# Kernel tuning notes

Measured on AMD Instinct MI355X. Metric: run time of the kernel, lower is better.

Reference implementation:

```python
import jax, jax.numpy as jnp
import numpy as np

DIM = 512
HEADS = 8
ALPHA = 0.5
HIDDEN = int(DIM * 2.0)
EPS = 1e-5


def _layernorm(x, g, b):
    mu = jnp.mean(x, axis=-1, keepdims=True)
    var = jnp.var(x, axis=-1, keepdims=True)
    return (x - mu) * jax.lax.rsqrt(var + EPS) * g + b


def setup_inputs() -> dict:
    key = jax.random.key(0)
    ks = jax.random.split(key, 8)
    B, N, C = 4, 1536, DIM
    s = lambda fan_in: 1.0 / np.sqrt(fan_in)
    return {
        "x": jax.random.normal(ks[0], (B, N, C), dtype=jnp.float32),
        "ln1_g": jnp.ones((C,), jnp.float32),
        "ln1_b": jnp.zeros((C,), jnp.float32),
        "qkv_w": jax.random.normal(ks[1], (C, 3 * C), jnp.float32) * s(C),
        "qkv_b": jnp.zeros((3 * C,), jnp.float32),
        "ln2_g": jnp.ones((C,), jnp.float32),
        "ln2_b": jnp.zeros((C,), jnp.float32),
        "fc1_w": jax.random.normal(ks[2], (C, HIDDEN), jnp.float32) * s(C),
        "fc1_b": jnp.zeros((HIDDEN,), jnp.float32),
        "fc2_w": jax.random.normal(ks[3], (HIDDEN, C), jnp.float32) * s(HIDDEN),
        "fc2_b": jnp.zeros((C,), jnp.float32),
    }


def reference(x, ln1_g, ln1_b, qkv_w, qkv_b, ln2_g, ln2_b, fc1_w, fc1_b, fc2_w, fc2_b):
    B, N, C = x.shape
    H = HEADS
    d = C // H
    S = N // 3

    h = _layernorm(x, ln1_g, ln1_b)
    qkv = (h @ qkv_w + qkv_b).reshape(B, N, 3, H, d)
    qkv = jnp.transpose(qkv, (2, 0, 3, 1, 4))  # [3,B,H,N,d]
    q, k, v = qkv[0], qkv[1], qkv[2]

    attn = jnp.einsum('bhnd,bhmd->bhnm', q, k) * (d ** -0.5)  # [B,H,N,N]
    # sequential cross-segment score mixing (matches in-place torch semantics)
    s0 = attn[:, :, 0:S]
    s1 = attn[:, :, S:2 * S] + ALPHA * s0
    s2 = attn[:, :, 2 * S:] + ALPHA * s1
    attn = jnp.concatenate([s0, s1, s2], axis=2)
    attn = jax.nn.softmax(attn, axis=-1)

    o = jnp.einsum('bhnm,bhmd->bhnd', attn, v)
    o = jnp.transpose(o, (0, 2, 1, 3)).reshape(B, N, C)
    x = x + o  # NOTE: self.proj is defined but unused in the original forward

    h2 = _layernorm(x, ln2_g, ln2_b)
    m = jax.nn.gelu(h2 @ fc1_w + fc1_b, approximate=False) @ fc2_w + fc2_b
    return x + m
```

## Files before the change

### kernel.cpp

```cpp
#include <hip/hip_runtime.h>
#include <hip/hip_bf16.h>
#include <math.h>

#define DIMC 512
#define NSEQ 1536
#define BATCH 4
#define NHEADS 8
#define HDIM 64
#define SSEG 512
#define HIDDEN_DIM 1024
#define ALPHA_C 0.5f
#define EPS_C 1e-5f
#define NROWS (BATCH*NSEQ)
#define SHIFT_L2 8.65617025f
#define HSHIFT_L2 4.328085125f
#define QSCALE_L2 0.18033688f

typedef __attribute__((ext_vector_type(8))) short bfrag8;
typedef __attribute__((ext_vector_type(8))) _Float16 hfrag8;
typedef __attribute__((ext_vector_type(2))) __fp16 h2;
typedef __attribute__((ext_vector_type(4))) float ffrag;
typedef float4 f4;


__device__ __forceinline__ ushort f2bf(float v) {
    __hip_bfloat16 hb = __float2bfloat16(v);
    return *(ushort*)&hb;
}

__device__ __forceinline__ void gl2lds16(const ushort* g, ushort* l) {
    __builtin_amdgcn_global_load_lds(
        (const __attribute__((address_space(1))) unsigned*)g,
        (__attribute__((address_space(3))) unsigned*)l, 16, 0, 0);
}

__global__ __launch_bounds__(256)
void prep_kernel(const float* __restrict__ qkv_w, const float* __restrict__ fc1_w,
                 const float* __restrict__ fc2_w, ushort* __restrict__ qkv_wt,
                 ushort* __restrict__ fc1_wt, ushort* __restrict__ fc2_wt,
                 const float* __restrict__ x, const float* __restrict__ g,
                 const float* __restrict__ bvec, ushort* __restrict__ h_out)
{
    int bid = blockIdx.x;
    if (bid < 448) {
        __shared__ float tile[64][65];
        const float* W; ushort* Wt; int K, N, n0, k0;
        if (bid < 192)      { W = qkv_w; Wt = qkv_wt; K = 512;  N = 1536; int b = bid;       n0 = (b % 24) * 64; k0 = (b / 24) * 64; }
        else if (bid < 320) { W = fc1_w; Wt = fc1_wt; K = 512;  N = 1024; int b = bid - 192; n0 = (b % 16) * 64; k0 = (b / 16) * 64; }
        else                { W = fc2_w; Wt = fc2_wt; K = 1024; N = 512;  int b = bid - 320; n0 = (b % 8)  * 64; k0 = (b / 8)  * 64; }
        int tx = threadIdx.x & 63, ty = threadIdx.x >> 6;
        #pragma unroll
        for (int i = 0; i < 16; i++) {
            int r = i * 4 + ty;
            tile[r][tx] = W[(size_t)(k0 + r) * N + n0 + tx];
        }
        __syncthreads();
        #pragma unroll
        for (int i = 0; i < 16; i++) {
            int r = i * 4 + ty;
            Wt[(size_t)(n0 + r) * K + k0 + tx] = f2bf(tile[tx][r]);
        }
    } else {
        __shared__ float red[16];
        int row = bid - 448;
        int t = threadIdx.x;
        int lane = t & 63, w = t >> 6;
        const float* rp = x + (size_t)row * DIMC;
        float v0 = rp[t];
        float v1 = rp[t + 256];
        float s = v0 + v1;
        float s2 = v0 * v0 + v1 * v1;
        #pragma unroll
        for (int o = 32; o > 0; o >>= 1) {
            s  += __shfl_down(s,  o, 64);
            s2 += __shfl_down(s2, o, 64);
        }
        if (lane == 0) { red[w] = s; red[8 + w] = s2; }
        __syncthreads();
        if (t == 0) {
            float a = red[0] + red[1] + red[2] + red[3];
            float c = red[8] + red[9] + red[10] + red[11];
            red[0] = a; red[8] = c;
        }
        __syncthreads();
        float mean = red[0] * (1.0f / DIMC);
        float var  = red[8] * (1.0f / DIMC) - mean * mean;
        float rstd = rsqrtf(var + EPS_C);
        ushort* op = h_out + (size_t)row * DIMC;
        op[t]       = f2bf((v0 - mean) * rstd * g[t]       + bvec[t]);
        op[t + 256] = f2bf((v1 - mean) * rstd * g[t + 256] + bvec[t + 256]);
    }
}

__global__ __launch_bounds__(256)
void ln_kernel(const float* __restrict__ in, const float* __restrict__ g,
               const float* __restrict__ b, ushort* __restrict__ out)
{
    __shared__ float red[16];
    int row = blockIdx.x;
    int t = threadIdx.x;
    int lane = t & 63, w = t >> 6;
    const float* rp = in + (size_t)row * DIMC;
    float v0 = rp[t];
    float v1 = rp[t + 256];
    float s = v0 + v1;
    float s2 = v0 * v0 + v1 * v1;
    #pragma unroll
    for (int o = 32; o > 0; o >>= 1) {
        s  += __shfl_down(s,  o, 64);
        s2 += __shfl_down(s2, o, 64);
    }
    if (lane == 0) { red[w] = s; red[8 + w] = s2; }
    __syncthreads();
    if (t == 0) {
        float a = red[0] + red[1] + red[2] + red[3];
        float c = red[8] + red[9] + red[10] + red[11];
        red[0] = a; red[8] = c;
    }
    __syncthreads();
    float mean = red[0] * (1.0f / DIMC);
    float var  = red[8] * (1.0f / DIMC) - mean * mean;
    float rstd = rsqrtf(var + EPS_C);
    ushort* op = out + (size_t)row * DIMC;
    op[t]       = f2bf((v0 - mean) * rstd * g[t]       + b[t]);
    op[t + 256] = f2bf((v1 - mean) * rstd * g[t + 256] + b[t + 256]);
}

template <int EPI>
__device__ __forceinline__
void mgemm_body(const ushort* __restrict__ A, const ushort* __restrict__ Wt,
                const float* __restrict__ bias, const float* resid,
                void* out, int M, int K, int Nn, int bx, int by,
                ushort* As, ushort* Bs)
{
    int tid = threadIdx.x;
    int lane = tid & 63, w = tid >> 6;
    int cl = lane & 15, qg = lane >> 4;
    int wm = w >> 1, wn = w & 1;
    int rowBase = by * 64, colBase = bx * 64;
    int sr = lane >> 2;
    int sb = (lane & 3) * 8;

    const ushort* agb = A  + (size_t)(rowBase + w * 16 + sr) * K + sb;
    const ushort* bgb = Wt + (size_t)(colBase + w * 16 + sr) * K + sb;

    ffrag acc[2][2];
    #pragma unroll
    for (int mi = 0; mi < 2; mi++)
        #pragma unroll
        for (int ni = 0; ni < 2; ni++)
            #pragma unroll
            for (int r = 0; r < 4; r++) acc[mi][ni][r] = 0.f;

    int niter = K >> 6;

    #pragma unroll
    for (int hf = 0; hf < 2; hf++) {
        gl2lds16(agb + hf * 32, As + (0 * 2 + hf) * 2048 + (w * 16) * 32);
        gl2lds16(bgb + hf * 32, Bs + (0 * 2 + hf) * 2048 + (w * 16) * 32);
    }
    __syncthreads();

    for (int it = 0; it < niter; it++) {
        int cur = it & 1;
        if (it + 1 < niter) {
            int k0 = (it + 1) * 64;
            #pragma unroll
            for (int hf = 0; hf < 2; hf++) {
                gl2lds16(agb + k0 + hf * 32, As + ((cur ^ 1) * 2 + hf) * 2048 + (w * 16) * 32);
                gl2lds16(bgb + k0 + hf * 32, Bs + ((cur ^ 1) * 2 + hf) * 2048 + (w * 16) * 32);
            }
        }
        #pragma unroll
        for (int ks = 0; ks < 2; ks++) {
            bfrag8 af[2], bf[2];
            #pragma unroll
            for (int mi = 0; mi < 2; mi++)
                af[mi] = *(const bfrag8*)&As[(cur * 2 + ks) * 2048 + (wm * 32 + mi * 16 + cl) * 32 + qg * 8];
            #pragma unroll
            for (int ni = 0; ni < 2; ni++)
                bf[ni] = *(const bfrag8*)&Bs[(cur * 2 + ks) * 2048 + (wn * 32 + ni * 16 + cl) * 32 + qg * 8];
            #pragma unroll
            for (int mi = 0; mi < 2; mi++)
                #pragma unroll
                for (int ni = 0; ni < 2; ni++)
                    acc[mi][ni] = __builtin_amdgcn_mfma_f32_16x16x32_bf16(af[mi], bf[ni], acc[mi][ni], 0, 0, 0);
        }
        if (it + 1 < niter) __syncthreads();
    }

    int bb = (EPI == 3) ? (colBase / 1536) : 0;

    #pragma unroll
    for (int mi = 0; mi < 2; mi++) {
        #pragma unroll
        for (int ni = 0; ni < 2; ni++) {
            #pragma unroll
            for (int r = 0; r < 4; r++) {
                int row = rowBase + wm * 32 + mi * 16 + qg * 4 + r;
                int col = colBase + wn * 32 + ni * 16 + cl;
                float v = acc[mi][ni][r] + (EPI == 3 ? bias[row] : bias[col]);
                if (EPI == 0 && col < DIMC) v *= QSCALE_L2;
                if (EPI == 1) v = 0.5f * v * (1.0f + erff(v * 0.70710678118654752f));
                if (EPI == 2) {
                    v += resid[(size_t)row * Nn + col];
                    ((float*)out)[(size_t)row * Nn + col] = v;
                } else if (EPI == 3) {
                    int t = col - bb * 1536;
                    int h = row >> 6, dl = row & 63;
                    int t32 = t & 31;
                    int slot = ((t32 & 15) >> 2) * 8 + (t32 >> 4) * 4 + (t32 & 3);
                    size_t a = ((size_t)(bb * 8 + h) * 48 + (t >> 5)) * 2048
                             + (dl >> 4) * 512 + (dl & 15) * 32 + slot;
                    _Float16 e = (_Float16)v;
                    ((ushort*)out)[a] = *(ushort*)&e;
                } else {
                    ((ushort*)out)[(size_t)row * Nn + col] = f2bf(v);
                }
            }
        }
    }
}

template <int EPI>
__device__ __forceinline__
void mgemm128_body(const ushort* __restrict__ A, const ushort* __restrict__ Wt,
                   const float* __restrict__ bias, void* out, void* out2,
                   int K, int Nn, int bx, int by,
                   ushort* As, ushort* Bs)
{
    int tid = threadIdx.x;
    int lane = tid & 63, w = tid >> 6;
    int cl = lane & 15, qg = lane >> 4;
    int wm = w >> 1, wn = w & 1;
    int rowBase = by * 64, colBase = bx * 128;
    int sr = lane >> 2;
    int sb = (lane & 3) * 8;

    const ushort* agb = A  + (size_t)(rowBase + w * 16 + sr) * K + sb;
    const ushort* bgb = Wt + (size_t)(colBase + w * 32 + sr) * K + sb;

    ffrag acc[2][4];
    #pragma unroll
    for (int mi = 0; mi < 2; mi++)
        #pragma unroll
        for (int ni = 0; ni < 4; ni++)
            #pragma unroll
            for (int r = 0; r < 4; r++) acc[mi][ni][r] = 0.f;

    int niter = K >> 6;

    #pragma unroll
    for (int hf = 0; hf < 2; hf++) {
        gl2lds16(agb + hf * 32,                  As + (0 * 2 + hf) * 2048 + (w * 16) * 32);
        gl2lds16(bgb + hf * 32,                  Bs + (0 * 2 + hf) * 4096 + (w * 32) * 32);
        gl2lds16(bgb + (size_t)16 * K + hf * 32, Bs + (0 * 2 + hf) * 4096 + (w * 32 + 16) * 32);
    }
    __syncthreads();

    for (int it = 0; it < niter; it++) {
        int cur = it & 1;
        if (it + 1 < niter) {
            int k0 = (it + 1) * 64;
            #pragma unroll
            for (int hf = 0; hf < 2; hf++) {
                gl2lds16(agb + k0 + hf * 32,                  As + ((cur ^ 1) * 2 + hf) * 2048 + (w * 16) * 32);
                gl2lds16(bgb + k0 + hf * 32,                  Bs + ((cur ^ 1) * 2 + hf) * 4096 + (w * 32) * 32);
                gl2lds16(bgb + (size_t)16 * K + k0 + hf * 32, Bs + ((cur ^ 1) * 2 + hf) * 4096 + (w * 32 + 16) * 32);
            }
        }
        #pragma unroll
        for (int ks = 0; ks < 2; ks++) {
            bfrag8 af[2], bf[4];
            #pragma unroll
            for (int mi = 0; mi < 2; mi++)
                af[mi] = *(const bfrag8*)&As[(cur * 2 + ks) * 2048 + (wm * 32 + mi * 16 + cl) * 32 + qg * 8];
            #pragma unroll
            for (int ni = 0; ni < 4; ni++)
                bf[ni] = *(const bfrag8*)&Bs[(cur * 2 + ks) * 4096 + (wn * 64 + ni * 16 + cl) * 32 + qg * 8];
            #pragma unroll
            for (int mi = 0; mi < 2; mi++)
                #pragma unroll
                for (int ni = 0; ni < 4; ni++)
                    acc[mi][ni] = __builtin_amdgcn_mfma_f32_16x16x32_bf16(af[mi], bf[ni], acc[mi][ni], 0, 0, 0);
        }
        if (it + 1 < niter) __syncthreads();
    }

    int bb = (EPI == 4) ? (rowBase / 1536) : 0;

    #pragma unroll
    for (int mi = 0; mi < 2; mi++) {
        #pragma unroll
        for (int ni = 0; ni < 4; ni++) {
            #pragma unroll
            for (int r = 0; r < 4; r++) {
                int row = rowBase + wm * 32 + mi * 16 + qg * 4 + r;
                int col = colBase + wn * 64 + ni * 16 + cl;
                float v = acc[mi][ni][r] + bias[col];
                if (EPI == 1) {
                    v = 0.5f * v * (1.0f + erff(v * 0.70710678118654752f));
                    ((ushort*)out)[(size_t)row * Nn + col] = f2bf(v);
                } else if (EPI == 4) {
                    int t = row - bb * 1536;
                    int h = (col >> 6) & 7;
                    int d = col & 63;
                    size_t a = ((size_t)(bb * 8 + h) * 96 + (t >> 4)) * 1024
                             + (d >> 5) * 512 + (t & 15) * 32 + (d & 31);
                    if (col < DIMC) {
                        v *= QSCALE_L2;
                        ((ushort*)out)[a] = f2bf(v);
                    } else {
                        ((ushort*)out2)[a] = f2bf(v);
                    }
                }
            }
        }
    }
}

template <int EPI>
__global__ __launch_bounds__(256)
void mgemm_kernel(const ushort* __restrict__ A, const ushort* __restrict__ Wt,
                  const float* __restrict__ bias, const float* resid,
                  void* out, int M, int K, int Nn)
{
    __shared__ ushort As[2 * 2 * 64 * 32];
    __shared__ ushort Bs[2 * 2 * 64 * 32];
    mgemm_body<EPI>(A, Wt, bias, resid, out, M, K, Nn, blockIdx.x, blockIdx.y, As, Bs);
}

template <int EPI>
__global__ __launch_bounds__(256)
void mgemm128_kernel(const ushort* __restrict__ A, const ushort* __restrict__ Wt,
                     const float* __restrict__ bias, void* out, int K, int Nn)
{
    __shared__ ushort As[2 * 2 * 64 * 32];
    __shared__ ushort Bs[2 * 2 * 128 * 32];
    mgemm128_body<EPI>(A, Wt, bias, out, nullptr, K, Nn, blockIdx.x, blockIdx.y, As, Bs);
}

__global__ __launch_bounds__(256)
void qkvt_kernel(const ushort* __restrict__ h_bf, const ushort* __restrict__ qkv_wt,
                 const float* __restrict__ qkv_b, ushort* __restrict__ qpk,
                 ushort* __restrict__ kpk, ushort* __restrict__ vpk)
{
    __shared__ ushort smem[2 * 2 * 192 * 32];
    int bid = blockIdx.x;
    if (bid < 768) {
        mgemm128_body<4>(h_bf, qkv_wt, qkv_b, (void*)qpk, (void*)kpk,
                         DIMC, 2 * DIMC, bid & 7, bid >> 3,
                         smem, smem + 2 * 2 * 64 * 32);
    } else {
        int b2 = bid - 768;
        mgemm_body<3>(qkv_wt + (size_t)2 * DIMC * DIMC, h_bf, qkv_b + 2 * DIMC, nullptr,
                      (void*)vpk, DIMC, DIMC, NROWS, b2 % 96, b2 / 96,
                      smem, smem + 2 * 2 * 64 * 32);
    }
}

__global__ __launch_bounds__(256)
void attn_kernel(const ushort* __restrict__ qpk, const ushort* __restrict__ kpk,
                 const ushort* __restrict__ vpk,
                 const float* __restrict__ x, float* __restrict__ xres)
{
    __shared__ float Op[48][68];
    __shared__ float Lp[4][4][16][3];

    int n = blockIdx.x + (blockIdx.y << 5);
    int idx = n >> 3;
    int bh  = (n & 7) * 4 + (idx & 3);
    int qi0 = (idx >> 2) * 16;
    int b = bh >> 3, h = bh & 7;
    int tid = threadIdx.x;
    int lane = tid & 63, w = tid >> 6;
    int cl = lane & 15, qg = lane >> 4;

    int lofs = cl * 32 + qg * 8;
    const ushort* qb = qpk + (size_t)bh * 96 * 1024;
    const ushort* kb = kpk + (size_t)bh * 96 * 1024;
    const ushort* vb = vpk + (size_t)bh * 48 * 2048;

    bfrag8 bq[3][2];
    #pragma unroll
    for (int seg = 0; seg < 3; seg++)
        #pragma unroll
        for (int f = 0; f < 2; f++)
            bq[seg][f] = *(const bfrag8*)&qb[(size_t)((seg * SSEG + qi0) >> 4) * 1024 + f * 512 + lofs];

    ffrag o[3][4];
    #pragma unroll
    for (int seg = 0; seg < 3; seg++)
        #pragma unroll
        for (int mg = 0; mg < 4; mg++)
            #pragma unroll
            for (int r = 0; r < 4; r++) o[seg][mg][r] = 0.f;
    float lp[3] = {0.f, 0.f, 0.f};

    h2 one2;
    one2[0] = (__fp16)1.0f; one2[1] = (__fp16)1.0f;

    int kb0 = w * 384;

    const ushort* kptr = kb + (size_t)(kb0 >> 4) * 1024 + lofs;
    const ushort* vptr = vb + (size_t)(kb0 >> 5) * 2048 + lofs;

    auto loadf = [&](hfrag8* av, bfrag8 (*af)[2]) {
        #pragma unroll
        for (int mg = 0; mg < 4; mg++)
            av[mg] = *(const hfrag8*)(vptr + mg * 512);
        vptr += 2048;
        #pragma unroll
        for (int s = 0; s < 2; s++)
            #pragma unroll
            for (int f = 0; f < 2; f++)
                af[s][f] = *(const bfrag8*)(kptr + s * 1024 + f * 512);
        kptr += 2048;
    };

    auto comp = [&](const hfrag8* av, const bfrag8 (*af)[2]) {
        ffrag c[2][3];
        #pragma unroll
        for (int s = 0; s < 2; s++) {
            #pragma unroll
            for (int r = 0; r < 4; r++) {
                c[s][0][r] = -SHIFT_L2;
                c[s][1][r] = -HSHIFT_L2;
                c[s][2][r] = -HSHIFT_L2;
            }
            #pragma unroll
            for (int seg = 0; seg < 3; seg++) {
                c[s][seg] = __builtin_amdgcn_mfma_f32_16x16x32_bf16(af[s][0], bq[seg][0], c[s][seg], 0, 0, 0);
                c[s][seg] = __builtin_amdgcn_mfma_f32_16x16x32_bf16(af[s][1], bq[seg][1], c[s][seg], 0, 0, 0);
            }
        }
        #pragma unroll
        for (int s = 0; s < 2; s++) {
            #pragma unroll
            for (int r = 0; r < 4; r++) {
                float sh0 = c[s][0][r];
                float sh1 = fmaf(ALPHA_C, sh0, c[s][1][r]);
                float sh2 = fmaf(ALPHA_C, sh1, c[s][2][r]);
                c[s][0][r] = __builtin_amdgcn_exp2f(sh0);
                c[s][1][r] = __builtin_amdgcn_exp2f(sh1);
                c[s][2][r] = __builtin_amdgcn_exp2f(sh2);
            }
        }
        #pragma unroll
        for (int seg = 0; seg < 3; seg++) {
            union { hfrag8 v8; h2 v2[4]; } u;
            u.v2[0] = __builtin_amdgcn_cvt_pkrtz(c[0][seg][0], c[0][seg][1]);
            u.v2[1] = __builtin_amdgcn_cvt_pkrtz(c[0][seg][2], c[0][seg][3]);
            u.v2[2] = __builtin_amdgcn_cvt_pkrtz(c[1][seg][0], c[1][seg][1]);
            u.v2[3] = __builtin_amdgcn_cvt_pkrtz(c[1][seg][2], c[1][seg][3]);
            lp[seg] = __builtin_amdgcn_fdot2(u.v2[0], one2, lp[seg], false);
            lp[seg] = __builtin_amdgcn_fdot2(u.v2[1], one2, lp[seg], false);
            lp[seg] = __builtin_amdgcn_fdot2(u.v2[2], one2, lp[seg], false);
            lp[seg] = __builtin_amdgcn_fdot2(u.v2[3], one2, lp[seg], false);
            #pragma unroll
            for (int mg = 0; mg < 4; mg++)
                o[seg][mg] = __builtin_amdgcn_mfma_f32_16x16x32_f16(av[mg], u.v8, o[seg][mg], 0, 0, 0);
        }
    };

    hfrag8 avA[4], avB[4];
    bfrag8 afA[2][2], afB[2][2];
    loadf(avA, afA);
    #pragma unroll 1
    for (int it = 0; it < 12; it += 2) {
        loadf(avB, afB);
        comp(avA, afA);
        if (it + 2 < 12) loadf(avA, afA);
        comp(avB, afB);
    }

    #pragma unroll
    for (int seg = 0; seg < 3; seg++) Lp[w][qg][cl][seg] = lp[seg];

    #pragma unroll 1
    for (int wv = 0; wv < 4; wv++) {
        __syncthreads();
        if (w == wv) {
            #pragma unroll
            for (int seg = 0; seg < 3; seg++)
                #pragma unroll
                for (int mg = 0; mg < 4; mg++) {
                    float* dst = &Op[seg * 16 + cl][mg * 16 + qg * 4];
                    if (wv == 0) {
                        #pragma unroll
                        for (int r = 0; r < 4; r++) dst[r] = o[seg][mg][r];
                    } else {
                        #pragma unroll
                        for (int r = 0; r < 4; r++) dst[r] += o[seg][mg][r];
                    }
                }
        }
    }
    __syncthreads();

    if (tid < 192) {
        int row = tid >> 2;
        int seg = row >> 4, q16 = row & 15;
        int d0 = (tid & 3) * 16;
        float l = 0.f;
        #pragma unroll
        for (int wv = 0; wv < 4; wv++)
            #pragma unroll
            for (int g2 = 0; g2 < 4; g2++)
                l += Lp[wv][g2][q16][seg];
        float invl = 1.0f / l;
        size_t rowg = ((size_t)(b * NSEQ + seg * SSEG + qi0 + q16)) * DIMC + h * HDIM + d0;
        #pragma unroll
        for (int dd = 0; dd < 16; dd += 4) {
            f4 xv = *(const f4*)(x + rowg + dd);
            f4 ov;
            ov.x = Op[row][d0 + dd + 0] * invl + xv.x;
            ov.y = Op[row][d0 + dd + 1] * invl + xv.y;
            ov.z = Op[row][d0 + dd + 2] * invl + xv.z;
            ov.w = Op[row][d0 + dd + 3] * invl + xv.w;
            *(f4*)(xres + rowg + dd) = ov;
        }
    }
}

extern "C" void kernel_launch(void* const* d_in, const int* in_sizes, int n_in,
                              void* d_out, int out_size, void* d_ws, size_t ws_size,
                              hipStream_t stream)
{
    const float* x     = (const float*)d_in[0];
    const float* ln1_g = (const float*)d_in[1];
    const float* ln1_b = (const float*)d_in[2];
    const float* qkv_w = (const float*)d_in[3];
    const float* qkv_b = (const float*)d_in[4];
    const float* ln2_g = (const float*)d_in[5];
    const float* ln2_b = (const float*)d_in[6];
    const float* fc1_w = (const float*)d_in[7];
    const float* fc1_b = (const float*)d_in[8];
    const float* fc2_w = (const float*)d_in[9];
    const float* fc2_b = (const float*)d_in[10];
    float* out = (float*)d_out;

    char* p = (char*)d_ws;
    ushort* h_bf    = (ushort*)p;  p += (size_t)NROWS * DIMC * 2;
    ushort* qpk     = (ushort*)p;  p += (size_t)32 * 96 * 1024 * 2;
    ushort* kpk     = (ushort*)p;  p += (size_t)32 * 96 * 1024 * 2;
    ushort* vpk     = (ushort*)p;  p += (size_t)32 * 48 * 2048 * 2;
    ushort* mid     = (ushort*)p;  p += (size_t)NROWS * HIDDEN_DIM * 2;
    ushort* qkv_wt  = (ushort*)p;  p += (size_t)3 * DIMC * DIMC * 2;
    ushort* fc1_wt  = (ushort*)p;  p += (size_t)HIDDEN_DIM * DIMC * 2;
    ushort* fc2_wt  = (ushort*)p;
    float* xres = out;

    prep_kernel<<<448 + NROWS, 256, 0, stream>>>(qkv_w, fc1_w, fc2_w, qkv_wt, fc1_wt, fc2_wt,
                                                 x, ln1_g, ln1_b, h_bf);

    qkvt_kernel<<<1536, 256, 0, stream>>>(h_bf, qkv_wt, qkv_b, qpk, kpk, vpk);

    attn_kernel<<<dim3(SSEG / 16, BATCH * NHEADS), 256, 0, stream>>>(qpk, kpk, vpk, x, xres);

    ln_kernel<<<NROWS, 256, 0, stream>>>(xres, ln2_g, ln2_b, h_bf);

    mgemm128_kernel<1><<<dim3(HIDDEN_DIM / 128, NROWS / 64), 256, 0, stream>>>(
        h_bf, fc1_wt, fc1_b, (void*)mid, DIMC, HIDDEN_DIM);

    mgemm_kernel<2><<<dim3(DIMC / 64, NROWS / 64), 256, 0, stream>>>(
        mid, fc2_wt, fc2_b, xres, (void*)out, NROWS, HIDDEN_DIM, DIMC);
}
```

Measured before the change: 190.9 us.

## Pre-tile GEMM operands into MFMA fragment layout and load directly to registers

Weights, layernorm outputs and the MLP hidden activations are now written in a 16x32 blocked layout that matches the MFMA fragment shape. The GEMMs then load fragments straight from global memory into registers with a two-stage software double buffer. This removes the LDS staging and the per-iteration barriers. The trade-off is that operand reuse across waves now relies on L1/L2 caching instead of shared memory, which may increase global traffic.

```diff
diff --git a/kernel.cpp b/kernel.cpp
--- a/kernel.cpp
+++ b/kernel.cpp
@@ -28,10 +28,50 @@
     return *(ushort*)&hb;
 }
 
-__device__ __forceinline__ void gl2lds16(const ushort* g, ushort* l) {
-    __builtin_amdgcn_global_load_lds(
-        (const __attribute__((address_space(1))) unsigned*)g,
-        (__attribute__((address_space(3))) unsigned*)l, 16, 0, 0);
+template <int NA, int NB>
+__device__ __forceinline__
+void sgemm_core(const ushort* __restrict__ A, const ushort* __restrict__ B,
+                int ra16, int cb16, int KB, int lofs, ffrag (&acc)[NA][NB])
+{
+    const ushort* ap[NA];
+    const ushort* bp[NB];
+    #pragma unroll
+    for (int i = 0; i < NA; i++) ap[i] = A + (size_t)(ra16 + i) * KB * 512 + lofs;
+    #pragma unroll
+    for (int j = 0; j < NB; j++) bp[j] = B + (size_t)(cb16 + j) * KB * 512 + lofs;
+    #pragma unroll
+    for (int i = 0; i < NA; i++)
+        #pragma unroll
+        for (int j = 0; j < NB; j++)
+            #pragma unroll
+            for (int r = 0; r < 4; r++) acc[i][j][r] = 0.f;
+
+    bfrag8 afA[NA], bfA[NB], afB[NA], bfB[NB];
+    auto ld = [&](bfrag8 (&af)[NA], bfrag8 (&bf)[NB]) {
+        #pragma unroll
+        for (int i = 0; i < NA; i++) { af[i] = *(const bfrag8*)ap[i]; ap[i] += 512; }
+        #pragma unroll
+        for (int j = 0; j < NB; j++) { bf[j] = *(const bfrag8*)bp[j]; bp[j] += 512; }
+    };
+    auto cmp = [&](const bfrag8 (&af)[NA], const bfrag8 (&bf)[NB]) {
+        #pragma unroll
+        for (int i = 0; i < NA; i++)
+            #pragma unroll
+            for (int j = 0; j < NB; j++)
+                acc[i][j] = __builtin_amdgcn_mfma_f32_16x16x32_bf16(af[i], bf[j], acc[i][j], 0, 0, 0);
+    };
+
+    ld(afA, bfA);
+    #pragma unroll 1
+    for (int kb = 2; kb < KB; kb += 2) {
+        ld(afB, bfB);
+        cmp(afA, bfA);
+        ld(afA, bfA);
+        cmp(afB, bfB);
+    }
+    ld(afB, bfB);
+    cmp(afA, bfA);
+    cmp(afB, bfB);
 }
 
 __global__ __launch_bounds__(256)
@@ -55,10 +95,13 @@
             tile[r][tx] = W[(size_t)(k0 + r) * N + n0 + tx];
         }
         __syncthreads();
+        int KB = K >> 5;
         #pragma unroll
         for (int i = 0; i < 16; i++) {
             int r = i * 4 + ty;
-            Wt[(size_t)(n0 + r) * K + k0 + tx] = f2bf(tile[tx][r]);
+            int n = n0 + r, k = k0 + tx;
+            Wt[((size_t)((n >> 4) * KB + (k >> 5))) * 512 + (n & 15) * 32 + (k & 31)]
+                = f2bf(tile[tx][r]);
         }
     } else {
         __shared__ float red[16];
@@ -86,9 +129,10 @@
         float mean = red[0] * (1.0f / DIMC);
         float var  = red[8] * (1.0f / DIMC) - mean * mean;
         float rstd = rsqrtf(var + EPS_C);
-        ushort* op = h_out + (size_t)row * DIMC;
-        op[t]       = f2bf((v0 - mean) * rstd * g[t]       + bvec[t]);
-        op[t + 256] = f2bf((v1 - mean) * rstd * g[t + 256] + bvec[t + 256]);
+        size_t rb = (size_t)(row >> 4) * 16 * 512 + (row & 15) * 32;
+        int t2 = t + 256;
+        h_out[rb + (t  >> 5) * 512 + (t  & 31)] = f2bf((v0 - mean) * rstd * g[t]  + bvec[t]);
+        h_out[rb + (t2 >> 5) * 512 + (t2 & 31)] = f2bf((v1 - mean) * rstd * g[t2] + bvec[t2]);
     }
 }
 
@@ -121,223 +165,10 @@
     float mean = red[0] * (1.0f / DIMC);
     float var  = red[8] * (1.0f / DIMC) - mean * mean;
     float rstd = rsqrtf(var + EPS_C);
-    ushort* op = out + (size_t)row * DIMC;
-    op[t]       = f2bf((v0 - mean) * rstd * g[t]       + b[t]);
-    op[t + 256] = f2bf((v1 - mean) * rstd * g[t + 256] + b[t + 256]);
-}
-
-template <int EPI>
-__device__ __forceinline__
-void mgemm_body(const ushort* __restrict__ A, const ushort* __restrict__ Wt,
-                const float* __restrict__ bias, const float* resid,
-                void* out, int M, int K, int Nn, int bx, int by,
-                ushort* As, ushort* Bs)
-{
-    int tid = threadIdx.x;
-    int lane = tid & 63, w = tid >> 6;
-    int cl = lane & 15, qg = lane >> 4;
-    int wm = w >> 1, wn = w & 1;
-    int rowBase = by * 64, colBase = bx * 64;
-    int sr = lane >> 2;
-    int sb = (lane & 3) * 8;
-
-    const ushort* agb = A  + (size_t)(rowBase + w * 16 + sr) * K + sb;
-    const ushort* bgb = Wt + (size_t)(colBase + w * 16 + sr) * K + sb;
-
-    ffrag acc[2][2];
-    #pragma unroll
-    for (int mi = 0; mi < 2; mi++)
-        #pragma unroll
-        for (int ni = 0; ni < 2; ni++)
-            #pragma unroll
-            for (int r = 0; r < 4; r++) acc[mi][ni][r] = 0.f;
-
-    int niter = K >> 6;
-
-    #pragma unroll
-    for (int hf = 0; hf < 2; hf++) {
-        gl2lds16(agb + hf * 32, As + (0 * 2 + hf) * 2048 + (w * 16) * 32);
-        gl2lds16(bgb + hf * 32, Bs + (0 * 2 + hf) * 2048 + (w * 16) * 32);
-    }
-    __syncthreads();
-
-    for (int it = 0; it < niter; it++) {
-        int cur = it & 1;
-        if (it + 1 < niter) {
-            int k0 = (it + 1) * 64;
-            #pragma unroll
-            for (int hf = 0; hf < 2; hf++) {
-                gl2lds16(agb + k0 + hf * 32, As + ((cur ^ 1) * 2 + hf) * 2048 + (w * 16) * 32);
-                gl2lds16(bgb + k0 + hf * 32, Bs + ((cur ^ 1) * 2 + hf) * 2048 + (w * 16) * 32);
-            }
-        }
-        #pragma unroll
-        for (int ks = 0; ks < 2; ks++) {
-            bfrag8 af[2], bf[2];
-            #pragma unroll
-            for (int mi = 0; mi < 2; mi++)
-                af[mi] = *(const bfrag8*)&As[(cur * 2 + ks) * 2048 + (wm * 32 + mi * 16 + cl) * 32 + qg * 8];
-            #pragma unroll
-            for (int ni = 0; ni < 2; ni++)
-                bf[ni] = *(const bfrag8*)&Bs[(cur * 2 + ks) * 2048 + (wn * 32 + ni * 16 + cl) * 32 + qg * 8];
-            #pragma unroll
-            for (int mi = 0; mi < 2; mi++)
-                #pragma unroll
-                for (int ni = 0; ni < 2; ni++)
-                    acc[mi][ni] = __builtin_amdgcn_mfma_f32_16x16x32_bf16(af[mi], bf[ni], acc[mi][ni], 0, 0, 0);
-        }
-        if (it + 1 < niter) __syncthreads();
-    }
-
-    int bb = (EPI == 3) ? (colBase / 1536) : 0;
-
-    #pragma unroll
-    for (int mi = 0; mi < 2; mi++) {
-        #pragma unroll
-        for (int ni = 0; ni < 2; ni++) {
-            #pragma unroll
-            for (int r = 0; r < 4; r++) {
-                int row = rowBase + wm * 32 + mi * 16 + qg * 4 + r;
-                int col = colBase + wn * 32 + ni * 16 + cl;
-                float v = acc[mi][ni][r] + (EPI == 3 ? bias[row] : bias[col]);
-                if (EPI == 0 && col < DIMC) v *= QSCALE_L2;
-                if (EPI == 1) v = 0.5f * v * (1.0f + erff(v * 0.70710678118654752f));
-                if (EPI == 2) {
-                    v += resid[(size_t)row * Nn + col];
-                    ((float*)out)[(size_t)row * Nn + col] = v;
-                } else if (EPI == 3) {
-                    int t = col - bb * 1536;
-                    int h = row >> 6, dl = row & 63;
-                    int t32 = t & 31;
-                    int slot = ((t32 & 15) >> 2) * 8 + (t32 >> 4) * 4 + (t32 & 3);
-                    size_t a = ((size_t)(bb * 8 + h) * 48 + (t >> 5)) * 2048
-                             + (dl >> 4) * 512 + (dl & 15) * 32 + slot;
-                    _Float16 e = (_Float16)v;
-                    ((ushort*)out)[a] = *(ushort*)&e;
-                } else {
-                    ((ushort*)out)[(size_t)row * Nn + col] = f2bf(v);
-                }
-            }
-        }
-    }
-}
-
-template <int EPI>
-__device__ __forceinline__
-void mgemm128_body(const ushort* __restrict__ A, const ushort* __restrict__ Wt,
-                   const float* __restrict__ bias, void* out, void* out2,
-                   int K, int Nn, int bx, int by,
-                   ushort* As, ushort* Bs)
-{
-    int tid = threadIdx.x;
-    int lane = tid & 63, w = tid >> 6;
-    int cl = lane & 15, qg = lane >> 4;
-    int wm = w >> 1, wn = w & 1;
-    int rowBase = by * 64, colBase = bx * 128;
-    int sr = lane >> 2;
-    int sb = (lane & 3) * 8;
-
-    const ushort* agb = A  + (size_t)(rowBase + w * 16 + sr) * K + sb;
-    const ushort* bgb = Wt + (size_t)(colBase + w * 32 + sr) * K + sb;
-
-    ffrag acc[2][4];
-    #pragma unroll
-    for (int mi = 0; mi < 2; mi++)
-        #pragma unroll
-        for (int ni = 0; ni < 4; ni++)
-            #pragma unroll
-            for (int r = 0; r < 4; r++) acc[mi][ni][r] = 0.f;
-
-    int niter = K >> 6;
-
-    #pragma unroll
-    for (int hf = 0; hf < 2; hf++) {
-        gl2lds16(agb + hf * 32,                  As + (0 * 2 + hf) * 2048 + (w * 16) * 32);
-        gl2lds16(bgb + hf * 32,                  Bs + (0 * 2 + hf) * 4096 + (w * 32) * 32);
-        gl2lds16(bgb + (size_t)16 * K + hf * 32, Bs + (0 * 2 + hf) * 4096 + (w * 32 + 16) * 32);
-    }
-    __syncthreads();
-
-    for (int it = 0; it < niter; it++) {
-        int cur = it & 1;
-        if (it + 1 < niter) {
-            int k0 = (it + 1) * 64;
-            #pragma unroll
-            for (int hf = 0; hf < 2; hf++) {
-                gl2lds16(agb + k0 + hf * 32,                  As + ((cur ^ 1) * 2 + hf) * 2048 + (w * 16) * 32);
-                gl2lds16(bgb + k0 + hf * 32,                  Bs + ((cur ^ 1) * 2 + hf) * 4096 + (w * 32) * 32);
-                gl2lds16(bgb + (size_t)16 * K + k0 + hf * 32, Bs + ((cur ^ 1) * 2 + hf) * 4096 + (w * 32 + 16) * 32);
-            }
-        }
-        #pragma unroll
-        for (int ks = 0; ks < 2; ks++) {
-            bfrag8 af[2], bf[4];
-            #pragma unroll
-            for (int mi = 0; mi < 2; mi++)
-                af[mi] = *(const bfrag8*)&As[(cur * 2 + ks) * 2048 + (wm * 32 + mi * 16 + cl) * 32 + qg * 8];
-            #pragma unroll
-            for (int ni = 0; ni < 4; ni++)
-                bf[ni] = *(const bfrag8*)&Bs[(cur * 2 + ks) * 4096 + (wn * 64 + ni * 16 + cl) * 32 + qg * 8];
-            #pragma unroll
-            for (int mi = 0; mi < 2; mi++)
-                #pragma unroll
-                for (int ni = 0; ni < 4; ni++)
-                    acc[mi][ni] = __builtin_amdgcn_mfma_f32_16x16x32_bf16(af[mi], bf[ni], acc[mi][ni], 0, 0, 0);
-        }
-        if (it + 1 < niter) __syncthreads();
-    }
-
-    int bb = (EPI == 4) ? (rowBase / 1536) : 0;
-
-    #pragma unroll
-    for (int mi = 0; mi < 2; mi++) {
-        #pragma unroll
-        for (int ni = 0; ni < 4; ni++) {
-            #pragma unroll
-            for (int r = 0; r < 4; r++) {
-                int row = rowBase + wm * 32 + mi * 16 + qg * 4 + r;
-                int col = colBase + wn * 64 + ni * 16 + cl;
-                float v = acc[mi][ni][r] + bias[col];
-                if (EPI == 1) {
-                    v = 0.5f * v * (1.0f + erff(v * 0.70710678118654752f));
-                    ((ushort*)out)[(size_t)row * Nn + col] = f2bf(v);
-                } else if (EPI == 4) {
-                    int t = row - bb * 1536;
-                    int h = (col >> 6) & 7;
-                    int d = col & 63;
-                    size_t a = ((size_t)(bb * 8 + h) * 96 + (t >> 4)) * 1024
-                             + (d >> 5) * 512 + (t & 15) * 32 + (d & 31);
-                    if (col < DIMC) {
-                        v *= QSCALE_L2;
-                        ((ushort*)out)[a] = f2bf(v);
-                    } else {
-                        ((ushort*)out2)[a] = f2bf(v);
-                    }
-                }
-            }
-        }
-    }
-}
-
-template <int EPI>
-__global__ __launch_bounds__(256)
-void mgemm_kernel(const ushort* __restrict__ A, const ushort* __restrict__ Wt,
-                  const float* __restrict__ bias, const float* resid,
-                  void* out, int M, int K, int Nn)
-{
-    __shared__ ushort As[2 * 2 * 64 * 32];
-    __shared__ ushort Bs[2 * 2 * 64 * 32];
-    mgemm_body<EPI>(A, Wt, bias, resid, out, M, K, Nn, blockIdx.x, blockIdx.y, As, Bs);
-}
-
-template <int EPI>
-__global__ __launch_bounds__(256)
-void mgemm128_kernel(const ushort* __restrict__ A, const ushort* __restrict__ Wt,
-                     const float* __restrict__ bias, void* out, int K, int Nn)
-{
-    __shared__ ushort As[2 * 2 * 64 * 32];
-    __shared__ ushort Bs[2 * 2 * 128 * 32];
-    mgemm128_body<EPI>(A, Wt, bias, out, nullptr, K, Nn, blockIdx.x, blockIdx.y, As, Bs);
+    size_t rb = (size_t)(row >> 4) * 16 * 512 + (row & 15) * 32;
+    int t2 = t + 256;
+    out[rb + (t  >> 5) * 512 + (t  & 31)] = f2bf((v0 - mean) * rstd * g[t]  + b[t]);
+    out[rb + (t2 >> 5) * 512 + (t2 & 31)] = f2bf((v1 - mean) * rstd * g[t2] + b[t2]);
 }
 
 __global__ __launch_bounds__(256)
@@ -345,18 +176,111 @@
                  const float* __restrict__ qkv_b, ushort* __restrict__ qpk,
                  ushort* __restrict__ kpk, ushort* __restrict__ vpk)
 {
-    __shared__ ushort smem[2 * 2 * 192 * 32];
+    int tid = threadIdx.x, lane = tid & 63, w = tid >> 6;
+    int cl = lane & 15, qg = lane >> 4;
+    int wm = w >> 1, wn = w & 1;
+    int lofs = cl * 32 + qg * 8;
     int bid = blockIdx.x;
+
     if (bid < 768) {
-        mgemm128_body<4>(h_bf, qkv_wt, qkv_b, (void*)qpk, (void*)kpk,
-                         DIMC, 2 * DIMC, bid & 7, bid >> 3,
-                         smem, smem + 2 * 2 * 64 * 32);
+        int r0 = (bid >> 3) * 64 + wm * 32;
+        int c0 = (bid & 7) * 128 + wn * 64;
+        ffrag acc[2][4];
+        sgemm_core<2, 4>(h_bf, qkv_wt, r0 >> 4, c0 >> 4, 16, lofs, acc);
+        int bb = r0 / 1536;
+        #pragma unroll
+        for (int mi = 0; mi < 2; mi++)
+            #pragma unroll
+            for (int ni = 0; ni < 4; ni++)
+                #pragma unroll
+                for (int r = 0; r < 4; r++) {
+                    int row = r0 + mi * 16 + qg * 4 + r;
+                    int col = c0 + ni * 16 + cl;
+                    float v = acc[mi][ni][r] + qkv_b[col];
+                    int t = row - bb * 1536;
+                    int h = (col >> 6) & 7, d = col & 63;
+                    size_t a = ((size_t)(bb * 8 + h) * 96 + (t >> 4)) * 1024
+                             + (d >> 5) * 512 + (t & 15) * 32 + (d & 31);
+                    if (col < DIMC) qpk[a] = f2bf(v * QSCALE_L2);
+                    else            kpk[a] = f2bf(v);
+                }
     } else {
         int b2 = bid - 768;
-        mgemm_body<3>(qkv_wt + (size_t)2 * DIMC * DIMC, h_bf, qkv_b + 2 * DIMC, nullptr,
-                      (void*)vpk, DIMC, DIMC, NROWS, b2 % 96, b2 / 96,
-                      smem, smem + 2 * 2 * 64 * 32);
-    }
+        int r0 = (b2 / 96) * 64 + wm * 32;
+        int c0 = (b2 % 96) * 64 + wn * 32;
+        ffrag acc[2][2];
+        sgemm_core<2, 2>(qkv_wt, h_bf, 64 + (r0 >> 4), c0 >> 4, 16, lofs, acc);
+        int bb = c0 / 1536;
+        #pragma unroll
+        for (int mi = 0; mi < 2; mi++)
+            #pragma unroll
+            for (int ni = 0; ni < 2; ni++)
+                #pragma unroll
+                for (int r = 0; r < 4; r++) {
+                    int row = r0 + mi * 16 + qg * 4 + r;
+                    int col = c0 + ni * 16 + cl;
+                    float v = acc[mi][ni][r] + qkv_b[1024 + row];
+                    int t = col - bb * 1536;
+                    int t32 = t & 31;
+                    int slot = ((t32 & 15) >> 2) * 8 + (t32 >> 4) * 4 + (t32 & 3);
+                    size_t a = ((size_t)(bb * 8 + (row >> 6)) * 48 + (t >> 5)) * 2048
+                             + ((row & 63) >> 4) * 512 + (row & 15) * 32 + slot;
+                    _Float16 e = (_Float16)v;
+                    vpk[a] = *(ushort*)&e;
+                }
+    }
+}
+
+__global__ __launch_bounds__(256)
+void fc1_kernel(const ushort* __restrict__ hin, const ushort* __restrict__ fc1_wt,
+                const float* __restrict__ fc1_b, ushort* __restrict__ mid)
+{
+    int tid = threadIdx.x, lane = tid & 63, w = tid >> 6;
+    int cl = lane & 15, qg = lane >> 4;
+    int wm = w >> 1, wn = w & 1;
+    int lofs = cl * 32 + qg * 8;
+    int r0 = blockIdx.y * 64 + wm * 32;
+    int c0 = blockIdx.x * 128 + wn * 64;
+    ffrag acc[2][4];
+    sgemm_core<2, 4>(hin, fc1_wt, r0 >> 4, c0 >> 4, 16, lofs, acc);
+    #pragma unroll
+    for (int mi = 0; mi < 2; mi++)
+        #pragma unroll
+        for (int ni = 0; ni < 4; ni++)
+            #pragma unroll
+            for (int r = 0; r < 4; r++) {
+                int row = r0 + mi * 16 + qg * 4 + r;
+                int col = c0 + ni * 16 + cl;
+                float v = acc[mi][ni][r] + fc1_b[col];
+                v = 0.5f * v * (1.0f + erff(v * 0.70710678118654752f));
+                mid[((size_t)((row >> 4) * 32 + (col >> 5))) * 512
+                    + (row & 15) * 32 + (col & 31)] = f2bf(v);
+            }
+}
+
+__global__ __launch_bounds__(256)
+void fc2_kernel(const ushort* __restrict__ mid, const ushort* __restrict__ fc2_wt,
+                const float* __restrict__ fc2_b, float* __restrict__ xres)
+{
+    int tid = threadIdx.x, lane = tid & 63, w = tid >> 6;
+    int cl = lane & 15, qg = lane >> 4;
+    int wm = w >> 1, wn = w & 1;
+    int lofs = cl * 32 + qg * 8;
+    int r0 = blockIdx.y * 64 + wm * 32;
+    int c0 = blockIdx.x * 64 + wn * 32;
+    ffrag acc[2][2];
+    sgemm_core<2, 2>(mid, fc2_wt, r0 >> 4, c0 >> 4, 32, lofs, acc);
+    #pragma unroll
+    for (int mi = 0; mi < 2; mi++)
+        #pragma unroll
+        for (int ni = 0; ni < 2; ni++)
+            #pragma unroll
+            for (int r = 0; r < 4; r++) {
+                int row = r0 + mi * 16 + qg * 4 + r;
+                int col = c0 + ni * 16 + cl;
+                size_t idx = (size_t)row * DIMC + col;
+                xres[idx] = acc[mi][ni][r] + fc2_b[col] + xres[idx];
+            }
 }
 
 __global__ __launch_bounds__(256)
@@ -560,9 +484,9 @@
 
     ln_kernel<<<NROWS, 256, 0, stream>>>(xres, ln2_g, ln2_b, h_bf);
 
-    mgemm128_kernel<1><<<dim3(HIDDEN_DIM / 128, NROWS / 64), 256, 0, stream>>>(
-        h_bf, fc1_wt, fc1_b, (void*)mid, DIMC, HIDDEN_DIM);
-
-    mgemm_kernel<2><<<dim3(DIMC / 64, NROWS / 64), 256, 0, stream>>>(
-        mid, fc2_wt, fc2_b, xres, (void*)out, NROWS, HIDDEN_DIM, DIMC);
-}
+    fc1_kernel<<<dim3(HIDDEN_DIM / 128, NROWS / 64), 256, 0, stream>>>(
+        h_bf, fc1_wt, fc1_b, mid);
+
+    fc2_kernel<<<dim3(DIMC / 64, NROWS / 64), 256, 0, stream>>>(
+        mid, fc2_wt, fc2_b, xres);
+}
```

Result: slower. 212.5 us (+11.3%).
